# Kernel tuning notes

Measured on AMD Instinct MI355X. Metric: run time of the kernel, lower is better.

Reference implementation:

```python
import jax, jax.numpy as jnp
import numpy as np

T = 5
EPS = 1e-5
NUM_CHANNELS = 256  # nc; g = C // nc


def setup_inputs() -> dict:
    key = jax.random.key(0)
    k1, k2, k3, k4 = jax.random.split(key, 4)
    B, C, H, W = 32, 256, 56, 56
    X = jax.random.normal(k1, (B, C, H, W), dtype=jnp.float32)
    running_rot = jax.random.normal(k2, (1, NUM_CHANNELS, NUM_CHANNELS), dtype=jnp.float32)
    weight = jax.random.uniform(k3, (1, C, 1, 1), dtype=jnp.float32)
    bias = jax.random.normal(k4, (1, C, 1, 1), dtype=jnp.float32)
    return {"X": X, "running_rot": running_rot, "weight": weight, "bias": bias}


def _iter_norm(X, nc, T, eps):
    # X: [B, C, H, W] -> x: [g, nc, m], m = B*H*W
    B, C, H, W = X.shape
    g = C // nc
    x = jnp.transpose(X, (1, 0, 2, 3)).reshape(g, nc, -1)
    m = x.shape[-1]
    mean = x.mean(-1, keepdims=True)
    xc = x - mean
    I = jnp.eye(nc, dtype=X.dtype)[None]                      # [1, nc, nc]
    Sigma = eps * I + jnp.matmul(xc, jnp.swapaxes(xc, 1, 2)) / m  # [g, nc, nc]
    rTr = 1.0 / jnp.einsum('gii->g', Sigma)[:, None, None]    # 1/trace(Sigma)
    Sigma_N = Sigma * rTr
    P = jnp.broadcast_to(I, (g, nc, nc))
    for _ in range(T):  # Newton-Schulz: P <- 1.5 P - 0.5 P^3 Sigma_N
        P = 1.5 * P - 0.5 * jnp.matmul(jnp.matmul(P, jnp.matmul(P, P)), Sigma_N)
    wm = P * jnp.sqrt(rTr)
    xn = jnp.matmul(wm, xc)                                   # [g, nc, m]
    Xn = jnp.transpose(xn.reshape(C, B, H, W), (1, 0, 2, 3))
    return Xn


def reference(X, running_rot, weight, bias):
    B, C, H, W = X.shape
    nc = NUM_CHANNELS
    g = C // nc
    Xn = _iter_norm(X, nc, T, EPS)                            # [B, C, H, W]
    Xh = Xn.reshape(B, g, nc, H, W)
    Xh = jnp.einsum('bgchw,gdc->bgdhw', Xh, running_rot)
    Xh = Xh.reshape(B, C, H, W)
    return Xh * weight + bias
```

## Files before the change

### kernel.cpp

```cpp
#include <hip/hip_runtime.h>

#define C_ 256
#define B_ 32
#define HW_ 3136
#define M_ 100352
#define NCHUNK_ 256
#define CHM_ 392
#define EPSV 1e-5f

typedef unsigned short ushort_t;
typedef unsigned int uint_t;
typedef __attribute__((ext_vector_type(8))) short short8v;
typedef __attribute__((ext_vector_type(16))) float f32x16;

__device__ __forceinline__ ushort_t bfhi(float v) {
    union { float f; uint_t u; } x; x.f = v;
    uint_t r = x.u + 0x7fffu + ((x.u >> 16) & 1u);
    return (ushort_t)(r >> 16);
}
__device__ __forceinline__ float bf2f(ushort_t b) {
    union { uint_t u; float f; } x; x.u = ((uint_t)b) << 16;
    return x.f;
}
__device__ __forceinline__ void bsplit(float v, ushort_t& h, ushort_t& l) {
    h = bfhi(v);
    l = bfhi(v - bf2f(h));
}

__global__ __launch_bounds__(1024) void k_gram(const float* __restrict__ X,
        float* __restrict__ pG, float* __restrict__ psum, float* __restrict__ pdiag,
        int NP, int atomic_mode) {
    __shared__ ushort_t xh[256 * 40];
    __shared__ ushort_t xl[256 * 40];
    __shared__ float red[1024];
    const int tid = threadIdx.x;
    const int wid = tid >> 6, lane = tid & 63;
    const int wr = wid >> 2, wc = wid & 3;
    const int lr = lane & 31, khalf = lane >> 5;
    const int sc = tid >> 2, skq = tid & 3;

    f32x16 acc[2][2];
#pragma unroll
    for (int ti = 0; ti < 2; ++ti)
#pragma unroll
        for (int tj = 0; tj < 2; ++tj)
#pragma unroll
            for (int r = 0; r < 16; ++r) acc[ti][tj][r] = 0.f;

    float csum = 0.f, cdiag = 0.f;

    const int chunk = blockIdx.x;
    const int b = chunk >> 3;
    const int hw0 = (chunk & 7) * CHM_;
    const float* Xb = X + (size_t)b * C_ * HW_ + hw0 + (size_t)sc * HW_ + 8 * skq;

    float4 cv0, cv1;
    {
        cv0 = *(const float4*)(Xb);
        cv1 = *(const float4*)(Xb + 4);
    }

    for (int k0 = 0; k0 < CHM_; k0 += 32) {
        float va[8] = {cv0.x, cv0.y, cv0.z, cv0.w, cv1.x, cv1.y, cv1.z, cv1.w};
        ushort_t h[8], l[8];
#pragma unroll
        for (int e = 0; e < 8; ++e) {
            csum += va[e]; cdiag += va[e] * va[e];
            bsplit(va[e], h[e], l[e]);
        }
        uint4 H, L;
        H.x = (uint_t)h[0] | ((uint_t)h[1] << 16); H.y = (uint_t)h[2] | ((uint_t)h[3] << 16);
        H.z = (uint_t)h[4] | ((uint_t)h[5] << 16); H.w = (uint_t)h[6] | ((uint_t)h[7] << 16);
        L.x = (uint_t)l[0] | ((uint_t)l[1] << 16); L.y = (uint_t)l[2] | ((uint_t)l[3] << 16);
        L.z = (uint_t)l[4] | ((uint_t)l[5] << 16); L.w = (uint_t)l[6] | ((uint_t)l[7] << 16);
        const int sel = sc * 40 + 8 * skq;
        *(uint4*)&xh[sel] = H;
        *(uint4*)&xl[sel] = L;
        __syncthreads();

        float4 nv0 = make_float4(0, 0, 0, 0), nv1 = nv0;
        const int kn = k0 + 32;
        if (kn < CHM_) {
            int klen = CHM_ - kn; if (klen > 32) klen = 32;
            if (8 * skq + 8 <= klen) {
                nv0 = *(const float4*)(Xb + kn);
                nv1 = *(const float4*)(Xb + kn + 4);
            }
        }

#pragma unroll
        for (int ik = 0; ik < 2; ++ik) {
            short8v ah[2], al[2], bh[2], bl[2];
#pragma unroll
            for (int t = 0; t < 2; ++t) {
                const int ea = (64 * wr + 32 * t + lr) * 40 + 16 * ik + 8 * khalf;
                ah[t] = *(const short8v*)&xh[ea];
                al[t] = *(const short8v*)&xl[ea];
                const int eb = (64 * wc + 32 * t + lr) * 40 + 16 * ik + 8 * khalf;
                bh[t] = *(const short8v*)&xh[eb];
                bl[t] = *(const short8v*)&xl[eb];
            }
#pragma unroll
            for (int ti = 0; ti < 2; ++ti)
#pragma unroll
                for (int tj = 0; tj < 2; ++tj) {
                    acc[ti][tj] = __builtin_amdgcn_mfma_f32_32x32x16_bf16(ah[ti], bh[tj], acc[ti][tj], 0, 0, 0);
                    acc[ti][tj] = __builtin_amdgcn_mfma_f32_32x32x16_bf16(ah[ti], bl[tj], acc[ti][tj], 0, 0, 0);
                    acc[ti][tj] = __builtin_amdgcn_mfma_f32_32x32x16_bf16(al[ti], bh[tj], acc[ti][tj], 0, 0, 0);
                }
        }
        __syncthreads();
        cv0 = nv0; cv1 = nv1;
    }

    const int p = atomic_mode ? (blockIdx.x % NP) : blockIdx.x;
    red[tid] = csum;
    __syncthreads();
    if (tid < C_) {
        float s = red[4 * tid] + red[4 * tid + 1] + red[4 * tid + 2] + red[4 * tid + 3];
        if (atomic_mode) atomicAdd(&psum[p * C_ + tid], s); else psum[p * C_ + tid] = s;
    }
    __syncthreads();
    red[tid] = cdiag;
    __syncthreads();
    if (tid < C_) {
        float s = red[4 * tid] + red[4 * tid + 1] + red[4 * tid + 2] + red[4 * tid + 3];
        if (atomic_mode) atomicAdd(&pdiag[p * C_ + tid], s); else pdiag[p * C_ + tid] = s;
    }

    float* og = pG + (size_t)p * 65536;
#pragma unroll
    for (int ti = 0; ti < 2; ++ti)
#pragma unroll
        for (int tj = 0; tj < 2; ++tj)
#pragma unroll
            for (int r = 0; r < 16; ++r) {
                const int rl = (r & 3) + 8 * (r >> 2) + 4 * khalf;
                const int row = 64 * wr + 32 * ti + rl;
                const int col = 64 * wc + 32 * tj + lr;
                if (atomic_mode) atomicAdd(&og[row * 256 + col], acc[ti][tj][r]);
                else og[row * 256 + col] = acc[ti][tj][r];
            }
}

__global__ __launch_bounds__(256) void k_stats(const float* __restrict__ psum,
        const float* __restrict__ pdiag, float* __restrict__ mean,
        float* __restrict__ scal, int NP) {
    __shared__ float red[256];
    const int c = threadIdx.x;
    float s = 0.f, d = 0.f;
    for (int p = 0; p < NP; ++p) { s += psum[p * C_ + c]; d += pdiag[p * C_ + c]; }
    const float mn = s * (1.f / (float)M_);
    mean[c] = mn;
    red[c] = d * (1.f / (float)M_) - mn * mn + EPSV;
    __syncthreads();
    for (int off = 128; off > 0; off >>= 1) {
        if (c < off) red[c] += red[c + off];
        __syncthreads();
    }
    if (c == 0) {
        float rTr = 1.f / red[0];
        scal[0] = rTr;
        scal[1] = sqrtf(rTr);
    }
}

__global__ __launch_bounds__(1024) void k_sigma(const float* __restrict__ pG,
        const float* __restrict__ mean, const float* __restrict__ scal,
        float* __restrict__ SigN, float* __restrict__ P, int NP) {
    const int e = blockIdx.x * 1024 + threadIdx.x;
    const int r = e >> 8, c = e & 255;
    float s = 0.f;
    for (int p = 0; p < NP; ++p) s += pG[(size_t)p * 65536 + e];
    float sig = s * (1.f / (float)M_) - mean[r] * mean[c] + ((r == c) ? EPSV : 0.f);
    float sn = sig * scal[0];
    SigN[e] = sn;
    P[e] = ((r == c) ? 1.5f : 0.f) - 0.5f * sn;
}

__device__ __forceinline__ void mm_body(const float* __restrict__ A,
        const float* __restrict__ Bm, int blk, int tid,
        float& a00, float& a01, float& a10, float& a11, int& row, int& col) {
    __shared__ __align__(16) float Ast[256][34];
    __shared__ __align__(16) float Bs[256][34];
    const int bi = blk >> 3, bj = blk & 7;
    const int i2 = tid >> 4, j2 = tid & 15;
#pragma unroll 4
    for (int s = 0; s < 32; ++s) {
        Ast[tid][s] = A[(32 * bi + s) * 256 + tid];
        int k = s * 8 + (tid >> 5), cc = tid & 31;
        Bs[k][cc] = Bm[k * 256 + 32 * bj + cc];
    }
    __syncthreads();
    a00 = 0.f; a01 = 0.f; a10 = 0.f; a11 = 0.f;
#pragma unroll 8
    for (int k = 0; k < 256; ++k) {
        float2 av = *(const float2*)&Ast[k][2 * i2];
        float2 bv = *(const float2*)&Bs[k][2 * j2];
        a00 += av.x * bv.x; a01 += av.x * bv.y;
        a10 += av.y * bv.x; a11 += av.y * bv.y;
    }
    row = 32 * bi + 2 * i2; col = 32 * bj + 2 * j2;
}

__global__ __launch_bounds__(256) void k_mm_pair(const float* __restrict__ A1,
        const float* __restrict__ B1, float* __restrict__ D1,
        const float* __restrict__ A2, const float* __restrict__ B2, float* __restrict__ D2) {
    const int second = blockIdx.x >> 6;
    const float* A = second ? A2 : A1;
    const float* Bm = second ? B2 : B1;
    float* D = second ? D2 : D1;
    float a00, a01, a10, a11; int row, col;
    mm_body(A, Bm, blockIdx.x & 63, threadIdx.x, a00, a01, a10, a11, row, col);
    D[row * 256 + col] = a00;       D[row * 256 + col + 1] = a01;
    D[(row + 1) * 256 + col] = a10; D[(row + 1) * 256 + col + 1] = a11;
}

__global__ __launch_bounds__(256) void k_mm_upd(const float* __restrict__ A,
        const float* __restrict__ Bm, float* __restrict__ P) {
    float a00, a01, a10, a11; int row, col;
    mm_body(A, Bm, blockIdx.x, threadIdx.x, a00, a01, a10, a11, row, col);
    int e0 = row * 256 + col, e1 = e0 + 256;
    P[e0]     = 1.5f * P[e0]     - 0.5f * a00;
    P[e0 + 1] = 1.5f * P[e0 + 1] - 0.5f * a01;
    P[e1]     = 1.5f * P[e1]     - 0.5f * a10;
    P[e1 + 1] = 1.5f * P[e1 + 1] - 0.5f * a11;
}

__global__ __launch_bounds__(256) void k_mm_rotM(const float* __restrict__ A,
        const float* __restrict__ Bm, float* __restrict__ Mf,
        ushort_t* __restrict__ Mhi, ushort_t* __restrict__ Mlo,
        const float* __restrict__ scal) {
    float a00, a01, a10, a11; int row, col;
    mm_body(A, Bm, blockIdx.x, threadIdx.x, a00, a01, a10, a11, row, col);
    const float sc = scal[1];
    float v[4] = {sc * a00, sc * a01, sc * a10, sc * a11};
    int idx[4] = {row * 256 + col, row * 256 + col + 1, (row + 1) * 256 + col, (row + 1) * 256 + col + 1};
#pragma unroll
    for (int e = 0; e < 4; ++e) {
        Mf[idx[e]] = v[e];
        ushort_t h, l; bsplit(v[e], h, l);
        Mhi[idx[e]] = h; Mlo[idx[e]] = l;
    }
}

__global__ __launch_bounds__(256) void k_beta(const float* __restrict__ Mf,
        const float* __restrict__ mean, const float* __restrict__ weight,
        const float* __restrict__ bias, float* __restrict__ beta) {
    const int d = threadIdx.x;
    float s = 0.f;
    for (int c = 0; c < C_; ++c) s += Mf[d * 256 + c] * mean[c];
    beta[d] = bias[d] - weight[d] * s;
}

__global__ __launch_bounds__(256) void k_out(const float* __restrict__ X,
        const ushort_t* __restrict__ Mhi, const ushort_t* __restrict__ Mlo,
        const float* __restrict__ weight, const float* __restrict__ beta,
        float* __restrict__ out) {
    __shared__ ushort_t Mh[128 * 40], Ml[128 * 40];
    __shared__ ushort_t Xh[128 * 40], Xl[128 * 40];
    __shared__ float wb[256];
    const int tid = threadIdx.x;
    const int wid = tid >> 6, lane = tid & 63;
    const int wr = wid >> 1, wc = wid & 1;
    const int lr = lane & 31, khalf = lane >> 5;

    const int bk = blockIdx.x;
    const int dh = bk & 1;
    const int tmp = bk >> 1;
    const int b = tmp / 25, kc = tmp - b * 25;
    const int d0 = dh * 128;
    const int hw0 = kc * 128;
    int klim = HW_ - hw0; if (klim > 128) klim = 128;

    const int md = tid >> 1, mh16 = tid & 1;
    const int cg = tid >> 5, kq = tid & 31;

    if (tid < 128) { wb[tid] = weight[d0 + tid]; wb[128 + tid] = beta[d0 + tid]; }

    f32x16 acc[2][2];
#pragma unroll
    for (int ti = 0; ti < 2; ++ti)
#pragma unroll
        for (int tj = 0; tj < 2; ++tj)
#pragma unroll
            for (int r = 0; r < 16; ++r) acc[ti][tj][r] = 0.f;

    const float* Xp = X + (size_t)b * C_ * HW_ + hw0 + 4 * kq;
    const bool xvalid = (4 * kq + 4 <= klim);

    uint4 pmh0, pmh1, pml0, pml1;
    float4 pxv[4];
    {
        const size_t mo = (size_t)(d0 + md) * 256 + 16 * mh16;
        pmh0 = *(const uint4*)&Mhi[mo]; pmh1 = *(const uint4*)&Mhi[mo + 8];
        pml0 = *(const uint4*)&Mlo[mo]; pml1 = *(const uint4*)&Mlo[mo + 8];
#pragma unroll
        for (int cc = 0; cc < 4; ++cc)
            pxv[cc] = xvalid ? *(const float4*)(Xp + (size_t)(4 * cg + cc) * HW_)
                             : make_float4(0, 0, 0, 0);
    }

    for (int step = 0; step < 8; ++step) {
        {
            const int me = md * 40 + 16 * mh16;
            *(uint4*)&Mh[me] = pmh0; *(uint4*)&Mh[me + 8] = pmh1;
            *(uint4*)&Ml[me] = pml0; *(uint4*)&Ml[me + 8] = pml1;
            ushort_t hx[4][4], lx[4][4];
#pragma unroll
            for (int cc = 0; cc < 4; ++cc) {
                float vv[4] = {pxv[cc].x, pxv[cc].y, pxv[cc].z, pxv[cc].w};
#pragma unroll
                for (int e = 0; e < 4; ++e) bsplit(vv[e], hx[cc][e], lx[cc][e]);
            }
#pragma unroll
            for (int e = 0; e < 4; ++e) {
                uint2 uh, ul;
                uh.x = (uint_t)hx[0][e] | ((uint_t)hx[1][e] << 16);
                uh.y = (uint_t)hx[2][e] | ((uint_t)hx[3][e] << 16);
                ul.x = (uint_t)lx[0][e] | ((uint_t)lx[1][e] << 16);
                ul.y = (uint_t)lx[2][e] | ((uint_t)lx[3][e] << 16);
                const int xe = (4 * kq + e) * 40 + 4 * cg;
                *(uint2*)&Xh[xe] = uh;
                *(uint2*)&Xl[xe] = ul;
            }
        }
        __syncthreads();

        if (step < 7) {
            const int c0 = 32 * (step + 1);
            const size_t mo = (size_t)(d0 + md) * 256 + c0 + 16 * mh16;
            pmh0 = *(const uint4*)&Mhi[mo]; pmh1 = *(const uint4*)&Mhi[mo + 8];
            pml0 = *(const uint4*)&Mlo[mo]; pml1 = *(const uint4*)&Mlo[mo + 8];
#pragma unroll
            for (int cc = 0; cc < 4; ++cc)
                pxv[cc] = xvalid ? *(const float4*)(Xp + (size_t)(c0 + 4 * cg + cc) * HW_)
                                 : make_float4(0, 0, 0, 0);
        }

#pragma unroll
        for (int ik = 0; ik < 2; ++ik) {
            short8v ah[2], al2[2], bh[2], bl[2];
#pragma unroll
            for (int t = 0; t < 2; ++t) {
                const int ea = (64 * wr + 32 * t + lr) * 40 + 16 * ik + 8 * khalf;
                ah[t]  = *(const short8v*)&Mh[ea];
                al2[t] = *(const short8v*)&Ml[ea];
                const int eb = (64 * wc + 32 * t + lr) * 40 + 16 * ik + 8 * khalf;
                bh[t] = *(const short8v*)&Xh[eb];
                bl[t] = *(const short8v*)&Xl[eb];
            }
#pragma unroll
            for (int ti = 0; ti < 2; ++ti)
#pragma unroll
                for (int tj = 0; tj < 2; ++tj) {
                    acc[ti][tj] = __builtin_amdgcn_mfma_f32_32x32x16_bf16(ah[ti],  bh[tj], acc[ti][tj], 0, 0, 0);
                    acc[ti][tj] = __builtin_amdgcn_mfma_f32_32x32x16_bf16(ah[ti],  bl[tj], acc[ti][tj], 0, 0, 0);
                    acc[ti][tj] = __builtin_amdgcn_mfma_f32_32x32x16_bf16(al2[ti], bh[tj], acc[ti][tj], 0, 0, 0);
                }
        }
        __syncthreads();
    }

#pragma unroll
    for (int ti = 0; ti < 2; ++ti)
#pragma unroll
        for (int tj = 0; tj < 2; ++tj)
#pragma unroll
            for (int r = 0; r < 16; ++r) {
                const int rl = (r & 3) + 8 * (r >> 2) + 4 * khalf;
                const int dl = 64 * wr + 32 * ti + rl;
                const int col = 64 * wc + 32 * tj + lr;
                if (col < klim) {
                    out[((size_t)b * C_ + d0 + dl) * HW_ + hw0 + col] =
                        wb[dl] * acc[ti][tj][r] + wb[128 + dl];
                }
            }
}

extern "C" void kernel_launch(void* const* d_in, const int* in_sizes, int n_in,
                              void* d_out, int out_size, void* d_ws, size_t ws_size,
                              hipStream_t stream) {
    const float* X      = (const float*)d_in[0];
    const float* rot    = (const float*)d_in[1];
    const float* weight = (const float*)d_in[2];
    const float* bias   = (const float*)d_in[3];
    float* out = (float*)d_out;
    float* wsf = (float*)d_ws;

    float* SigN = wsf;
    float* P    = wsf + 65536;
    float* P2   = wsf + 2 * 65536;
    float* Q    = wsf + 3 * 65536;
    float* Mf   = wsf + 4 * 65536;
    ushort_t* Mhi = (ushort_t*)(wsf + 5 * 65536);
    ushort_t* Mlo = (ushort_t*)(wsf + 5 * 65536 + 32768);
    float* mean = wsf + 6 * 65536;
    float* beta = mean + 256;
    float* scal = mean + 512;
    float* psum = mean + 768;

    long avail = (long)(ws_size / 4) - (6L * 65536 + 768);
    int NP = (int)(avail / (65536 + 512));
    int atomic_mode = 0;
    if (NP >= 256) {
        NP = 256;
    } else {
        if (NP < 1) NP = 1;
        atomic_mode = 1;
    }
    float* pdiag = psum + (size_t)NP * 256;
    float* pG    = pdiag + (size_t)NP * 256;

    if (atomic_mode) {
        hipMemsetAsync(psum, 0, ((size_t)NP * 512 + (size_t)NP * 65536) * 4, stream);
    }

    k_gram<<<256, 1024, 0, stream>>>(X, pG, psum, pdiag, NP, atomic_mode);
    k_stats<<<1, 256, 0, stream>>>(psum, pdiag, mean, scal, NP);
    k_sigma<<<64, 1024, 0, stream>>>(pG, mean, scal, SigN, P, NP);
    for (int it = 0; it < 4; ++it) {
        k_mm_pair<<<128, 256, 0, stream>>>(P, P, P2, P, SigN, Q);
        k_mm_upd<<<64, 256, 0, stream>>>(P2, Q, P);
    }
    k_mm_rotM<<<64, 256, 0, stream>>>(rot, P, Mf, Mhi, Mlo, scal);
    k_beta<<<1, 256, 0, stream>>>(Mf, mean, weight, bias, beta);
    k_out<<<1600, 256, 0, stream>>>(X, Mhi, Mlo, weight, beta, out);
}
```

Baseline: 504.0 us.

## Pre-split X into bf16 hi/lo planes and stream Gram tiles via global_load_lds

A new k_split kernel converts X once into channel-major bf16 hi/lo planes, stored in the output buffer as scratch, and emits per-chunk channel sums and sums of squares. k_gram then reads those planes through direct global-to-LDS 16-byte loads into a double-buffered, XOR-swizzled LDS layout, using 224 blocks of 7 chunks each and dropping the atomic fallback. k_out is retiled to 64-column blocks that cover all 256 output channels, loads M through global_load_lds and transposes X into swizzled LDS. The cost is an extra write and read pass over 2x bf16 copies of X, plus a larger partial-Gram reduction in k_sigma, traded for less per-block conversion work and better load overlap.

```diff
diff --git a/kernel.cpp b/kernel.cpp
--- a/kernel.cpp
+++ b/kernel.cpp
@@ -4,9 +4,10 @@
 #define B_ 32
 #define HW_ 3136
 #define M_ 100352
-#define NCHUNK_ 256
-#define CHM_ 392
 #define EPSV 1e-5f
+#define GBLK 224
+#define GCH 7
+#define NPART 1568
 
 typedef unsigned short ushort_t;
 typedef unsigned int uint_t;
@@ -27,17 +28,58 @@
     l = bfhi(v - bf2f(h));
 }
 
-__global__ __launch_bounds__(1024) void k_gram(const float* __restrict__ X,
-        float* __restrict__ pG, float* __restrict__ psum, float* __restrict__ pdiag,
-        int NP, int atomic_mode) {
-    __shared__ ushort_t xh[256 * 40];
-    __shared__ ushort_t xl[256 * 40];
-    __shared__ float red[1024];
+__device__ __forceinline__ void gl_lds16(const void* g, void* l) {
+    __builtin_amdgcn_global_load_lds(
+        (const __attribute__((address_space(1))) unsigned int*)g,
+        (__attribute__((address_space(3))) unsigned int*)l, 16, 0, 0);
+}
+
+__global__ __launch_bounds__(256) void k_split(const float* __restrict__ X,
+        ushort_t* __restrict__ Xh, ushort_t* __restrict__ Xl,
+        float* __restrict__ psum, float* __restrict__ pdiag) {
+    const int tid = threadIdx.x;
+    const int c_l = tid >> 3, h = tid & 7;
+    const int c = blockIdx.z * 32 + c_l;
+    const int hw = blockIdx.x * 64 + h * 8;
+    const float* src = X + ((size_t)(blockIdx.y * C_ + c) * HW_ + hw);
+    float4 v0 = *(const float4*)src;
+    float4 v1 = *(const float4*)(src + 4);
+    float va[8] = {v0.x, v0.y, v0.z, v0.w, v1.x, v1.y, v1.z, v1.w};
+    ushort_t hh[8], ll[8];
+    float s = 0.f, q = 0.f;
+#pragma unroll
+    for (int e = 0; e < 8; ++e) {
+        s += va[e]; q += va[e] * va[e];
+        bsplit(va[e], hh[e], ll[e]);
+    }
+    uint4 H, L;
+    H.x = (uint_t)hh[0] | ((uint_t)hh[1] << 16); H.y = (uint_t)hh[2] | ((uint_t)hh[3] << 16);
+    H.z = (uint_t)hh[4] | ((uint_t)hh[5] << 16); H.w = (uint_t)hh[6] | ((uint_t)hh[7] << 16);
+    L.x = (uint_t)ll[0] | ((uint_t)ll[1] << 16); L.y = (uint_t)ll[2] | ((uint_t)ll[3] << 16);
+    L.z = (uint_t)ll[4] | ((uint_t)ll[5] << 16); L.w = (uint_t)ll[6] | ((uint_t)ll[7] << 16);
+    const size_t o = (size_t)c * M_ + (size_t)blockIdx.y * HW_ + hw;
+    *(uint4*)&Xh[o] = H;
+    *(uint4*)&Xl[o] = L;
+#pragma unroll
+    for (int off = 1; off < 8; off <<= 1) {
+        s += __shfl_xor(s, off);
+        q += __shfl_xor(q, off);
+    }
+    if (h == 0) {
+        const int p = blockIdx.y * 49 + blockIdx.x;
+        psum[p * C_ + c] = s;
+        pdiag[p * C_ + c] = q;
+    }
+}
+
+__global__ __launch_bounds__(1024) void k_gram(const ushort_t* __restrict__ Xh,
+        const ushort_t* __restrict__ Xl, float* __restrict__ pG) {
+    __shared__ ushort_t buf[2][2][C_ * 64];
     const int tid = threadIdx.x;
     const int wid = tid >> 6, lane = tid & 63;
     const int wr = wid >> 2, wc = wid & 3;
     const int lr = lane & 31, khalf = lane >> 5;
-    const int sc = tid >> 2, skq = tid & 3;
+    const int sr = lane >> 3, sq = lane & 7;
 
     f32x16 acc[2][2];
 #pragma unroll
@@ -47,58 +89,38 @@
 #pragma unroll
             for (int r = 0; r < 16; ++r) acc[ti][tj][r] = 0.f;
 
-    float csum = 0.f, cdiag = 0.f;
-
-    const int chunk = blockIdx.x;
-    const int b = chunk >> 3;
-    const int hw0 = (chunk & 7) * CHM_;
-    const float* Xb = X + (size_t)b * C_ * HW_ + hw0 + (size_t)sc * HW_ + 8 * skq;
-
-    float4 cv0, cv1;
-    {
-        cv0 = *(const float4*)(Xb);
-        cv1 = *(const float4*)(Xb + 4);
-    }
-
-    for (int k0 = 0; k0 < CHM_; k0 += 32) {
-        float va[8] = {cv0.x, cv0.y, cv0.z, cv0.w, cv1.x, cv1.y, cv1.z, cv1.w};
-        ushort_t h[8], l[8];
-#pragma unroll
-        for (int e = 0; e < 8; ++e) {
-            csum += va[e]; cdiag += va[e] * va[e];
-            bsplit(va[e], h[e], l[e]);
-        }
-        uint4 H, L;
-        H.x = (uint_t)h[0] | ((uint_t)h[1] << 16); H.y = (uint_t)h[2] | ((uint_t)h[3] << 16);
-        H.z = (uint_t)h[4] | ((uint_t)h[5] << 16); H.w = (uint_t)h[6] | ((uint_t)h[7] << 16);
-        L.x = (uint_t)l[0] | ((uint_t)l[1] << 16); L.y = (uint_t)l[2] | ((uint_t)l[3] << 16);
-        L.z = (uint_t)l[4] | ((uint_t)l[5] << 16); L.w = (uint_t)l[6] | ((uint_t)l[7] << 16);
-        const int sel = sc * 40 + 8 * skq;
-        *(uint4*)&xh[sel] = H;
-        *(uint4*)&xl[sel] = L;
-        __syncthreads();
-
-        float4 nv0 = make_float4(0, 0, 0, 0), nv1 = nv0;
-        const int kn = k0 + 32;
-        if (kn < CHM_) {
-            int klen = CHM_ - kn; if (klen > 32) klen = 32;
-            if (8 * skq + 8 <= klen) {
-                nv0 = *(const float4*)(Xb + kn);
-                nv1 = *(const float4*)(Xb + kn + 4);
-            }
-        }
-
-#pragma unroll
-        for (int ik = 0; ik < 2; ++ik) {
+    const int chunk0 = blockIdx.x * GCH;
+
+    auto stage = [&](int bb, int ch) {
+        const size_t m0 = (size_t)ch * 64;
+#pragma unroll
+        for (int s = 0; s < 2; ++s) {
+            const ushort_t* src = s ? Xl : Xh;
+#pragma unroll
+            for (int i = 0; i < 2; ++i) {
+                const int r0 = wid * 16 + i * 8;
+                const int r = r0 + sr;
+                gl_lds16(src + (size_t)r * M_ + m0 + 8 * (sq ^ (r & 7)),
+                         &buf[bb][s][r0 * 64]);
+            }
+        }
+    };
+
+    auto compute = [&](int bb) {
+#pragma unroll
+        for (int ik = 0; ik < 4; ++ik) {
+            const int q0 = 2 * ik + khalf;
             short8v ah[2], al[2], bh[2], bl[2];
 #pragma unroll
             for (int t = 0; t < 2; ++t) {
-                const int ea = (64 * wr + 32 * t + lr) * 40 + 16 * ik + 8 * khalf;
-                ah[t] = *(const short8v*)&xh[ea];
-                al[t] = *(const short8v*)&xl[ea];
-                const int eb = (64 * wc + 32 * t + lr) * 40 + 16 * ik + 8 * khalf;
-                bh[t] = *(const short8v*)&xh[eb];
-                bl[t] = *(const short8v*)&xl[eb];
+                const int ra = 64 * wr + 32 * t + lr;
+                const int ia = ra * 64 + 8 * (q0 ^ (ra & 7));
+                ah[t] = *(const short8v*)&buf[bb][0][ia];
+                al[t] = *(const short8v*)&buf[bb][1][ia];
+                const int rb = 64 * wc + 32 * t + lr;
+                const int ib = rb * 64 + 8 * (q0 ^ (rb & 7));
+                bh[t] = *(const short8v*)&buf[bb][0][ib];
+                bl[t] = *(const short8v*)&buf[bb][1][ib];
             }
 #pragma unroll
             for (int ti = 0; ti < 2; ++ti)
@@ -109,26 +131,16 @@
                     acc[ti][tj] = __builtin_amdgcn_mfma_f32_32x32x16_bf16(al[ti], bh[tj], acc[ti][tj], 0, 0, 0);
                 }
         }
+    };
+
+    stage(0, chunk0);
+    for (int t = 0; t < GCH; ++t) {
         __syncthreads();
-        cv0 = nv0; cv1 = nv1;
-    }
-
-    const int p = atomic_mode ? (blockIdx.x % NP) : blockIdx.x;
-    red[tid] = csum;
-    __syncthreads();
-    if (tid < C_) {
-        float s = red[4 * tid] + red[4 * tid + 1] + red[4 * tid + 2] + red[4 * tid + 3];
-        if (atomic_mode) atomicAdd(&psum[p * C_ + tid], s); else psum[p * C_ + tid] = s;
-    }
-    __syncthreads();
-    red[tid] = cdiag;
-    __syncthreads();
-    if (tid < C_) {
-        float s = red[4 * tid] + red[4 * tid + 1] + red[4 * tid + 2] + red[4 * tid + 3];
-        if (atomic_mode) atomicAdd(&pdiag[p * C_ + tid], s); else pdiag[p * C_ + tid] = s;
-    }
-
-    float* og = pG + (size_t)p * 65536;
+        if (t + 1 < GCH) stage((t + 1) & 1, chunk0 + t + 1);
+        compute(t & 1);
+    }
+
+    float* og = pG + (size_t)blockIdx.x * 65536;
 #pragma unroll
     for (int ti = 0; ti < 2; ++ti)
 #pragma unroll
@@ -138,18 +150,36 @@
                 const int rl = (r & 3) + 8 * (r >> 2) + 4 * khalf;
                 const int row = 64 * wr + 32 * ti + rl;
                 const int col = 64 * wc + 32 * tj + lr;
-                if (atomic_mode) atomicAdd(&og[row * 256 + col], acc[ti][tj][r]);
-                else og[row * 256 + col] = acc[ti][tj][r];
-            }
-}
-
-__global__ __launch_bounds__(256) void k_stats(const float* __restrict__ psum,
-        const float* __restrict__ pdiag, float* __restrict__ mean,
-        float* __restrict__ scal, int NP) {
+                og[row * 256 + col] = acc[ti][tj][r];
+            }
+}
+
+__global__ __launch_bounds__(256) void k_red1(const float* __restrict__ psum,
+        const float* __restrict__ pdiag, float* __restrict__ rsum,
+        float* __restrict__ rdiag) {
+    const int c = threadIdx.x, g = blockIdx.x;
+    float s = 0.f, d = 0.f;
+#pragma unroll 4
+    for (int b = 0; b < 32; ++b) {
+        const size_t p = (size_t)(b * 49 + g) * C_ + c;
+        s += psum[p];
+        d += pdiag[p];
+    }
+    rsum[g * C_ + c] = s;
+    rdiag[g * C_ + c] = d;
+}
+
+__global__ __launch_bounds__(256) void k_stats(const float* __restrict__ rsum,
+        const float* __restrict__ rdiag, float* __restrict__ mean,
+        float* __restrict__ scal) {
     __shared__ float red[256];
     const int c = threadIdx.x;
     float s = 0.f, d = 0.f;
-    for (int p = 0; p < NP; ++p) { s += psum[p * C_ + c]; d += pdiag[p * C_ + c]; }
+#pragma unroll 7
+    for (int p = 0; p < 49; ++p) {
+        s += rsum[p * C_ + c];
+        d += rdiag[p * C_ + c];
+    }
     const float mn = s * (1.f / (float)M_);
     mean[c] = mn;
     red[c] = d * (1.f / (float)M_) - mn * mn + EPSV;
@@ -165,13 +195,16 @@
     }
 }
 
-__global__ __launch_bounds__(1024) void k_sigma(const float* __restrict__ pG,
+__global__ __launch_bounds__(256) void k_sigma(const float* __restrict__ pG,
         const float* __restrict__ mean, const float* __restrict__ scal,
-        float* __restrict__ SigN, float* __restrict__ P, int NP) {
-    const int e = blockIdx.x * 1024 + threadIdx.x;
+        float* __restrict__ SigN, float* __restrict__ P) {
+    const int e = blockIdx.x * 256 + threadIdx.x;
     const int r = e >> 8, c = e & 255;
     float s = 0.f;
-    for (int p = 0; p < NP; ++p) s += pG[(size_t)p * 65536 + e];
+    for (int p = 0; p < GBLK; p += 4) {
+        s += pG[(size_t)p * 65536 + e] + pG[(size_t)(p + 1) * 65536 + e]
+           + pG[(size_t)(p + 2) * 65536 + e] + pG[(size_t)(p + 3) * 65536 + e];
+    }
     float sig = s * (1.f / (float)M_) - mean[r] * mean[c] + ((r == c) ? EPSV : 0.f);
     float sn = sig * scal[0];
     SigN[e] = sn;
@@ -257,26 +290,15 @@
         const ushort_t* __restrict__ Mhi, const ushort_t* __restrict__ Mlo,
         const float* __restrict__ weight, const float* __restrict__ beta,
         float* __restrict__ out) {
-    __shared__ ushort_t Mh[128 * 40], Ml[128 * 40];
-    __shared__ ushort_t Xh[128 * 40], Xl[128 * 40];
-    __shared__ float wb[256];
+    __shared__ ushort_t Mh[C_ * 64], Ml[C_ * 64];
+    __shared__ ushort_t Th[64 * 64], Tl[64 * 64];
     const int tid = threadIdx.x;
     const int wid = tid >> 6, lane = tid & 63;
-    const int wr = wid >> 1, wc = wid & 1;
     const int lr = lane & 31, khalf = lane >> 5;
-
-    const int bk = blockIdx.x;
-    const int dh = bk & 1;
-    const int tmp = bk >> 1;
-    const int b = tmp / 25, kc = tmp - b * 25;
-    const int d0 = dh * 128;
-    const int hw0 = kc * 128;
-    int klim = HW_ - hw0; if (klim > 128) klim = 128;
-
-    const int md = tid >> 1, mh16 = tid & 1;
-    const int cg = tid >> 5, kq = tid & 31;
-
-    if (tid < 128) { wb[tid] = weight[d0 + tid]; wb[128 + tid] = beta[d0 + tid]; }
+    const int sr = lane >> 3, sq = lane & 7;
+    const int cpair = tid >> 3, h = tid & 7;
+    const int hw0 = blockIdx.x * 64;
+    const int b = blockIdx.y;
 
     f32x16 acc[2][2];
 #pragma unroll
@@ -286,80 +308,63 @@
 #pragma unroll
             for (int r = 0; r < 16; ++r) acc[ti][tj][r] = 0.f;
 
-    const float* Xp = X + (size_t)b * C_ * HW_ + hw0 + 4 * kq;
-    const bool xvalid = (4 * kq + 4 <= klim);
-
-    uint4 pmh0, pmh1, pml0, pml1;
-    float4 pxv[4];
-    {
-        const size_t mo = (size_t)(d0 + md) * 256 + 16 * mh16;
-        pmh0 = *(const uint4*)&Mhi[mo]; pmh1 = *(const uint4*)&Mhi[mo + 8];
-        pml0 = *(const uint4*)&Mlo[mo]; pml1 = *(const uint4*)&Mlo[mo + 8];
-#pragma unroll
-        for (int cc = 0; cc < 4; ++cc)
-            pxv[cc] = xvalid ? *(const float4*)(Xp + (size_t)(4 * cg + cc) * HW_)
-                             : make_float4(0, 0, 0, 0);
-    }
-
-    for (int step = 0; step < 8; ++step) {
-        {
-            const int me = md * 40 + 16 * mh16;
-            *(uint4*)&Mh[me] = pmh0; *(uint4*)&Mh[me + 8] = pmh1;
-            *(uint4*)&Ml[me] = pml0; *(uint4*)&Ml[me + 8] = pml1;
-            ushort_t hx[4][4], lx[4][4];
-#pragma unroll
-            for (int cc = 0; cc < 4; ++cc) {
-                float vv[4] = {pxv[cc].x, pxv[cc].y, pxv[cc].z, pxv[cc].w};
-#pragma unroll
-                for (int e = 0; e < 4; ++e) bsplit(vv[e], hx[cc][e], lx[cc][e]);
-            }
-#pragma unroll
-            for (int e = 0; e < 4; ++e) {
-                uint2 uh, ul;
-                uh.x = (uint_t)hx[0][e] | ((uint_t)hx[1][e] << 16);
-                uh.y = (uint_t)hx[2][e] | ((uint_t)hx[3][e] << 16);
-                ul.x = (uint_t)lx[0][e] | ((uint_t)lx[1][e] << 16);
-                ul.y = (uint_t)lx[2][e] | ((uint_t)lx[3][e] << 16);
-                const int xe = (4 * kq + e) * 40 + 4 * cg;
-                *(uint2*)&Xh[xe] = uh;
-                *(uint2*)&Xl[xe] = ul;
-            }
+    const float* Xb = X + (size_t)(b * C_) * HW_ + hw0;
+
+    for (int c0 = 0; c0 < C_; c0 += 64) {
+        const int ca = c0 + 2 * cpair;
+        float xa[2][8];
+#pragma unroll
+        for (int e = 0; e < 8; ++e) {
+            xa[0][e] = Xb[(size_t)ca * HW_ + h + 8 * e];
+            xa[1][e] = Xb[(size_t)(ca + 1) * HW_ + h + 8 * e];
         }
         __syncthreads();
-
-        if (step < 7) {
-            const int c0 = 32 * (step + 1);
-            const size_t mo = (size_t)(d0 + md) * 256 + c0 + 16 * mh16;
-            pmh0 = *(const uint4*)&Mhi[mo]; pmh1 = *(const uint4*)&Mhi[mo + 8];
-            pml0 = *(const uint4*)&Mlo[mo]; pml1 = *(const uint4*)&Mlo[mo + 8];
-#pragma unroll
-            for (int cc = 0; cc < 4; ++cc)
-                pxv[cc] = xvalid ? *(const float4*)(Xp + (size_t)(c0 + 4 * cg + cc) * HW_)
-                                 : make_float4(0, 0, 0, 0);
-        }
-
-#pragma unroll
-        for (int ik = 0; ik < 2; ++ik) {
-            short8v ah[2], al2[2], bh[2], bl[2];
+#pragma unroll
+        for (int s = 0; s < 2; ++s) {
+            const ushort_t* msrc = s ? Mlo : Mhi;
+            ushort_t* mdst = s ? Ml : Mh;
+#pragma unroll
+            for (int i = 0; i < 8; ++i) {
+                const int r0 = wid * 64 + i * 8;
+                const int r = r0 + sr;
+                gl_lds16(msrc + (size_t)r * C_ + c0 + 8 * (sq ^ (r & 7)), &mdst[r0 * 64]);
+            }
+        }
+#pragma unroll
+        for (int e = 0; e < 8; ++e) {
+            const int row = h + 8 * e;
+            ushort_t h0, l0, h1, l1;
+            bsplit(xa[0][e], h0, l0);
+            bsplit(xa[1][e], h1, l1);
+            const int ui = row * 64 + 8 * ((cpair >> 2) ^ h) + 2 * (cpair & 3);
+            *(uint_t*)&Th[ui] = (uint_t)h0 | ((uint_t)h1 << 16);
+            *(uint_t*)&Tl[ui] = (uint_t)l0 | ((uint_t)l1 << 16);
+        }
+        __syncthreads();
+#pragma unroll
+        for (int ik = 0; ik < 4; ++ik) {
+            const int q0 = 2 * ik + khalf;
+            short8v ah[2], am[2], bh[2], bl[2];
 #pragma unroll
             for (int t = 0; t < 2; ++t) {
-                const int ea = (64 * wr + 32 * t + lr) * 40 + 16 * ik + 8 * khalf;
-                ah[t]  = *(const short8v*)&Mh[ea];
-                al2[t] = *(const short8v*)&Ml[ea];
-                const int eb = (64 * wc + 32 * t + lr) * 40 + 16 * ik + 8 * khalf;
-                bh[t] = *(const short8v*)&Xh[eb];
-                bl[t] = *(const short8v*)&Xl[eb];
+                const int ra = 64 * wid + 32 * t + lr;
+                const int ia = ra * 64 + 8 * (q0 ^ (ra & 7));
+                ah[t] = *(const short8v*)&Mh[ia];
+                am[t] = *(const short8v*)&Ml[ia];
+                const int rb = 32 * t + lr;
+                const int ib = rb * 64 + 8 * (q0 ^ (rb & 7));
+                bh[t] = *(const short8v*)&Th[ib];
+                bl[t] = *(const short8v*)&Tl[ib];
             }
 #pragma unroll
             for (int ti = 0; ti < 2; ++ti)
 #pragma unroll
                 for (int tj = 0; tj < 2; ++tj) {
-                    acc[ti][tj] = __builtin_amdgcn_mfma_f32_32x32x16_bf16(ah[ti],  bh[tj], acc[ti][tj], 0, 0, 0);
-                    acc[ti][tj] = __builtin_amdgcn_mfma_f32_32x32x16_bf16(ah[ti],  bl[tj], acc[ti][tj], 0, 0, 0);
-                    acc[ti][tj] = __builtin_amdgcn_mfma_f32_32x32x16_bf16(al2[ti], bh[tj], acc[ti][tj], 0, 0, 0);
+                    acc[ti][tj] = __builtin_amdgcn_mfma_f32_32x32x16_bf16(ah[ti], bh[tj], acc[ti][tj], 0, 0, 0);
+                    acc[ti][tj] = __builtin_amdgcn_mfma_f32_32x32x16_bf16(ah[ti], bl[tj], acc[ti][tj], 0, 0, 0);
+                    acc[ti][tj] = __builtin_amdgcn_mfma_f32_32x32x16_bf16(am[ti], bh[tj], acc[ti][tj], 0, 0, 0);
                 }
         }
-        __syncthreads();
     }
 
 #pragma unroll
@@ -369,12 +374,10 @@
 #pragma unroll
             for (int r = 0; r < 16; ++r) {
                 const int rl = (r & 3) + 8 * (r >> 2) + 4 * khalf;
-                const int dl = 64 * wr + 32 * ti + rl;
-                const int col = 64 * wc + 32 * tj + lr;
-                if (col < klim) {
-                    out[((size_t)b * C_ + d0 + dl) * HW_ + hw0 + col] =
-                        wb[dl] * acc[ti][tj][r] + wb[128 + dl];
-                }
+                const int d = 64 * wid + 32 * ti + rl;
+                const int col = 32 * tj + lr;
+                out[((size_t)(b * C_ + d)) * HW_ + hw0 + col] =
+                    weight[d] * acc[ti][tj][r] + beta[d];
             }
 }
 
@@ -388,42 +391,36 @@
     float* out = (float*)d_out;
     float* wsf = (float*)d_ws;
 
+    ushort_t* Xh = (ushort_t*)d_out;
+    ushort_t* Xl = Xh + (size_t)C_ * M_;
+
     float* SigN = wsf;
     float* P    = wsf + 65536;
     float* P2   = wsf + 2 * 65536;
     float* Q    = wsf + 3 * 65536;
     float* Mf   = wsf + 4 * 65536;
     ushort_t* Mhi = (ushort_t*)(wsf + 5 * 65536);
-    ushort_t* Mlo = (ushort_t*)(wsf + 5 * 65536 + 32768);
-    float* mean = wsf + 6 * 65536;
-    float* beta = mean + 256;
-    float* scal = mean + 512;
-    float* psum = mean + 768;
-
-    long avail = (long)(ws_size / 4) - (6L * 65536 + 768);
-    int NP = (int)(avail / (65536 + 512));
-    int atomic_mode = 0;
-    if (NP >= 256) {
-        NP = 256;
-    } else {
-        if (NP < 1) NP = 1;
-        atomic_mode = 1;
-    }
-    float* pdiag = psum + (size_t)NP * 256;
-    float* pG    = pdiag + (size_t)NP * 256;
-
-    if (atomic_mode) {
-        hipMemsetAsync(psum, 0, ((size_t)NP * 512 + (size_t)NP * 65536) * 4, stream);
-    }
-
-    k_gram<<<256, 1024, 0, stream>>>(X, pG, psum, pdiag, NP, atomic_mode);
-    k_stats<<<1, 256, 0, stream>>>(psum, pdiag, mean, scal, NP);
-    k_sigma<<<64, 1024, 0, stream>>>(pG, mean, scal, SigN, P, NP);
+    ushort_t* Mlo = Mhi + 65536;
+    float* small = wsf + 6 * 65536;
+    float* mean  = small;
+    float* betav = small + 256;
+    float* scal  = small + 512;
+    float* psum  = small + 1024;
+    float* pdiag = psum + (size_t)NPART * C_;
+    float* rsum  = pdiag + (size_t)NPART * C_;
+    float* rdiag = rsum + 49 * C_;
+    float* pG    = rdiag + 49 * C_;
+
+    k_split<<<dim3(49, 32, 8), 256, 0, stream>>>(X, Xh, Xl, psum, pdiag);
+    k_gram<<<GBLK, 1024, 0, stream>>>(Xh, Xl, pG);
+    k_red1<<<49, 256, 0, stream>>>(psum, pdiag, rsum, rdiag);
+    k_stats<<<1, 256, 0, stream>>>(rsum, rdiag, mean, scal);
+    k_sigma<<<256, 256, 0, stream>>>(pG, mean, scal, SigN, P);
     for (int it = 0; it < 4; ++it) {
         k_mm_pair<<<128, 256, 0, stream>>>(P, P, P2, P, SigN, Q);
         k_mm_upd<<<64, 256, 0, stream>>>(P2, Q, P);
     }
     k_mm_rotM<<<64, 256, 0, stream>>>(rot, P, Mf, Mhi, Mlo, scal);
-    k_beta<<<1, 256, 0, stream>>>(Mf, mean, weight, bias, beta);
-    k_out<<<1600, 256, 0, stream>>>(X, Mhi, Mlo, weight, beta, out);
-}
+    k_beta<<<1, 256, 0, stream>>>(Mf, mean, weight, bias, betav);
+    k_out<<<dim3(49, 32), 256, 0, stream>>>(X, Mhi, Mlo, weight, betav, out);
+}
```

After: 425.0 us. 15.7% less time.
